# Kernel optimization log

Hardware: AMD Instinct MI355X
Metric: run time of the kernel (lower is better)

The kernel has to match this reference:

```python
import jax, jax.numpy as jnp
import numpy as np

N_NODES = 100000
N_EDGES = 1600000
D_IN = 128
D_OUT = 128
LN_EPS = 1e-5
MEAN_EPS = 1e-8


def setup_inputs() -> dict:
    key = jax.random.key(0)
    ks = jax.random.split(key, 8)
    x = jax.random.normal(ks[0], (N_NODES, D_IN), dtype=jnp.float32)
    edge_index = jax.random.randint(ks[1], (2, N_EDGES), 0, N_NODES, dtype=jnp.int64)
    s = 1.0 / np.sqrt(D_IN)
    W_agg = jax.random.uniform(ks[2], (D_OUT, D_IN), jnp.float32, -s, s)
    b_agg = jax.random.uniform(ks[3], (D_OUT,), jnp.float32, -s, s)
    W_self = jax.random.uniform(ks[4], (D_OUT, D_IN), jnp.float32, -s, s)
    b_self = jax.random.uniform(ks[5], (D_OUT,), jnp.float32, -s, s)
    gamma = jnp.ones((D_OUT,), jnp.float32)
    beta = jnp.zeros((D_OUT,), jnp.float32)
    return {"x": x, "edge_index": edge_index, "W_agg": W_agg, "b_agg": b_agg,
            "W_self": W_self, "b_self": b_self, "gamma": gamma, "beta": beta}


def reference(x, edge_index, W_agg, b_agg, W_self, b_self, gamma, beta):
    row, col = edge_index[0], edge_index[1]
    num_nodes = x.shape[0]
    # self path: Linear(in, out)
    self_out = x @ W_self.T + b_self                              # [N, D_OUT]
    # mean aggregation: fused gather + segment-sum (no index_add buffer passes)
    neighbor_sum = jax.ops.segment_sum(x[col], row, num_segments=num_nodes)   # [N, D_IN]
    ones = jnp.ones((col.shape[0], 1), dtype=x.dtype)
    neighbor_count = jax.ops.segment_sum(ones, row, num_segments=num_nodes)   # [N, 1]
    neighbor_mean = neighbor_sum / (neighbor_count + MEAN_EPS)
    agg_out = neighbor_mean @ W_agg.T + b_agg                     # [N, D_OUT]
    # relu -> LayerNorm (dropout is identity at eval)
    h = jax.nn.relu(self_out + agg_out)
    mu = jnp.mean(h, axis=-1, keepdims=True)
    var = jnp.mean(jnp.square(h - mu), axis=-1, keepdims=True)
    return (h - mu) * jax.lax.rsqrt(var + LN_EPS) * gamma + beta
```

## Files before the change

kernel.cpp:

```cpp
#include <hip/hip_runtime.h>

#define N_NODES 100000
#define N_EDGES 1600000
#define D 128
#define RPB 64
#define NBUCKET 1563
#define NBLK 196
#define EPB 8192
#define AGG_CAP 2048
#define XCB 3125
#define SCAN_PAD 1792

constexpr float LN_EPS   = 1e-5f;
constexpr float MEAN_EPS = 1e-8f;

typedef __attribute__((ext_vector_type(8))) short bf16x8;
typedef __attribute__((ext_vector_type(4))) float f32x4;
typedef __attribute__((ext_vector_type(2))) float f32x2;
typedef __attribute__((ext_vector_type(4))) unsigned uint4e;
typedef __attribute__((ext_vector_type(2))) unsigned uint2e;

__device__ inline unsigned short f2bf(float f) {
  union { float f; unsigned u; } v; v.f = f;
  return (unsigned short)((v.u + 0x7FFFu + ((v.u >> 16) & 1u)) >> 16);
}
__device__ inline unsigned pack2(float a, float b) {
  return (unsigned)f2bf(a) | ((unsigned)f2bf(b) << 16);
}

__global__ __launch_bounds__(256) void prep_sort(
    const float* __restrict__ x, const int* __restrict__ ei,
    const float* __restrict__ Wself, const float* __restrict__ Wagg,
    const float* __restrict__ bself, const float* __restrict__ bagg,
    unsigned short* __restrict__ xb, unsigned char* __restrict__ x8,
    unsigned short* __restrict__ wcat, float* __restrict__ bsum,
    unsigned* __restrict__ ent_sorted, int* __restrict__ chunkoff) {
  __shared__ int ent_s[EPB];
  __shared__ int cnt_s[SCAN_PAD];
  __shared__ int off_s[SCAN_PAD];
  __shared__ int sb[256];
  const int bid = blockIdx.x;
  const int t = threadIdx.x;

  if (bid < NBLK) {
    const int ebase = bid * EPB;
    const int nch = min(EPB, N_EDGES - ebase);
    const int base4 = bid * (EPB / 4);
    const int end4 = base4 + (nch >> 2);

    for (int i = t; i < SCAN_PAD; i += 256) cnt_s[i] = 0;
    __syncthreads();

#pragma unroll
    for (int k = 0; k < EPB / 1024; ++k) {
      int i4 = base4 + k * 256 + t;
      if (i4 < end4) {
        int4 r = ((const int4*)ei)[i4];
        atomicAdd(&cnt_s[r.x >> 6], 1);
        atomicAdd(&cnt_s[r.y >> 6], 1);
        atomicAdd(&cnt_s[r.z >> 6], 1);
        atomicAdd(&cnt_s[r.w >> 6], 1);
      }
    }
    __syncthreads();

    int psum = 0;
#pragma unroll
    for (int i = 0; i < 7; ++i) psum += cnt_s[t * 7 + i];
    sb[t] = psum;
    __syncthreads();
    for (int off = 1; off < 256; off <<= 1) {
      int u = (t >= off) ? sb[t - off] : 0;
      __syncthreads();
      sb[t] += u;
      __syncthreads();
    }
    int run = sb[t] - psum;
#pragma unroll
    for (int i = 0; i < 7; ++i) {
      off_s[t * 7 + i] = run;
      run += cnt_s[t * 7 + i];
    }
    __syncthreads();

    for (int b = t; b < NBUCKET; b += 256)
      chunkoff[b * NBLK + bid] = off_s[b] | (cnt_s[b] << 14);
    __syncthreads();

#pragma unroll
    for (int k = 0; k < EPB / 1024; ++k) {
      int i4 = base4 + k * 256 + t;
      if (i4 < end4) {
        int4 r = ((const int4*)ei)[i4];
        int4 c = ((const int4*)(ei + N_EDGES))[i4];
        int p0 = atomicAdd(&off_s[r.x >> 6], 1);
        ent_s[p0] = ((r.x & 63) << 17) | c.x;
        int p1 = atomicAdd(&off_s[r.y >> 6], 1);
        ent_s[p1] = ((r.y & 63) << 17) | c.y;
        int p2 = atomicAdd(&off_s[r.z >> 6], 1);
        ent_s[p2] = ((r.z & 63) << 17) | c.z;
        int p3 = atomicAdd(&off_s[r.w >> 6], 1);
        ent_s[p3] = ((r.w & 63) << 17) | c.w;
      }
    }
    __syncthreads();

    for (int i = t; i < nch; i += 256)
      ent_sorted[ebase + i] = (unsigned)ent_s[i];
  } else if (bid < NBLK + XCB) {
    const int f = (bid - NBLK) * 4096 + t * 16;
    const float4 v0 = ((const float4*)x)[(f >> 2) + 0];
    const float4 v1 = ((const float4*)x)[(f >> 2) + 1];
    const float4 v2 = ((const float4*)x)[(f >> 2) + 2];
    const float4 v3 = ((const float4*)x)[(f >> 2) + 3];
    uint4e lo, hi;
    lo.x = pack2(v0.x, v0.y); lo.y = pack2(v0.z, v0.w);
    lo.z = pack2(v1.x, v1.y); lo.w = pack2(v1.z, v1.w);
    hi.x = pack2(v2.x, v2.y); hi.y = pack2(v2.z, v2.w);
    hi.z = pack2(v3.x, v3.y); hi.w = pack2(v3.z, v3.w);
    *(uint4e*)(xb + f) = lo;
    *(uint4e*)(xb + f + 8) = hi;
    unsigned q0 = 0, q1 = 0, q2 = 0, q3 = 0;
    q0 = __builtin_amdgcn_cvt_pk_fp8_f32(v0.x, v0.y, q0, false);
    q0 = __builtin_amdgcn_cvt_pk_fp8_f32(v0.z, v0.w, q0, true);
    q1 = __builtin_amdgcn_cvt_pk_fp8_f32(v1.x, v1.y, q1, false);
    q1 = __builtin_amdgcn_cvt_pk_fp8_f32(v1.z, v1.w, q1, true);
    q2 = __builtin_amdgcn_cvt_pk_fp8_f32(v2.x, v2.y, q2, false);
    q2 = __builtin_amdgcn_cvt_pk_fp8_f32(v2.z, v2.w, q2, true);
    q3 = __builtin_amdgcn_cvt_pk_fp8_f32(v3.x, v3.y, q3, false);
    q3 = __builtin_amdgcn_cvt_pk_fp8_f32(v3.z, v3.w, q3, true);
    uint4e q; q.x = q0; q.y = q1; q.z = q2; q.w = q3;
    *(uint4e*)(x8 + f) = q;
  } else {
    const int blk = bid - NBLK - XCB;
#pragma unroll
    for (int k = 0; k < 8; ++k) {
      int idx = blk * 2048 + k * 256 + t;
      int o = idx >> 8, kc = idx & 255;
      float v = (kc < 128) ? Wself[o * 128 + kc] : Wagg[o * 128 + (kc - 128)];
      wcat[o * 256 + kc] = f2bf(v);
    }
    if (blk == 0 && t < 128) bsum[t] = bself[t] + bagg[t];
    if (blk == 0 && t < 32)
      *(unsigned*)(x8 + (size_t)N_NODES * 128 + t * 4) = 0u;
  }
}

__global__ __launch_bounds__(256) void aggregate(
    const unsigned char* __restrict__ x8, const unsigned* __restrict__ ent_sorted,
    const int* __restrict__ chunkoff, float* out) {
  __shared__ int ent_s[AGG_CAP];
  __shared__ int col_s[AGG_CAP];
  __shared__ int cnt_s[RPB];
  __shared__ int off_s[RPB];
  __shared__ int cur_s[RPB];
  __shared__ int wsum[4];

  const int b = blockIdx.x;
  const int t = threadIdx.x;
  const int w = t >> 6, lane = t & 63;

  int beg = 0, len = 0;
  if (t < NBLK) {
    int pk = chunkoff[b * NBLK + t];
    beg = pk & 16383;
    len = pk >> 14;
  }
  int v = len;
#pragma unroll
  for (int off = 1; off < 64; off <<= 1) {
    int u = __shfl_up(v, off, 64);
    if (lane >= off) v += u;
  }
  if (lane == 63) wsum[w] = v;
  if (t < RPB) cnt_s[t] = 0;
  __syncthreads();
  int pre = 0;
  for (int i = 0; i < w; ++i) pre += wsum[i];
  int n = wsum[0] + wsum[1] + wsum[2] + wsum[3];
  if (n > AGG_CAP) n = AGG_CAP;
  int dst = pre + v - len;
  if (t < NBLK) {
    const unsigned* src = ent_sorted + t * EPB + beg;
    for (int i = 0; i < len; ++i)
      if (dst + i < AGG_CAP) ent_s[dst + i] = (int)src[i];
  }
  __syncthreads();

  for (int i = t; i < n; i += 256) atomicAdd(&cnt_s[ent_s[i] >> 17], 1);
  __syncthreads();

  if (t < RPB) {
    int c = cnt_s[t];
    int sv = c;
#pragma unroll
    for (int off = 1; off < 64; off <<= 1) {
      int u = __shfl_up(sv, off, 64);
      if (t >= off) sv += u;
    }
    off_s[t] = sv - c;
    cur_s[t] = sv - c;
  }
  __syncthreads();

  for (int i = t; i < n; i += 256) {
    int e = ent_s[i];
    int pos = atomicAdd(&cur_s[e >> 17], 1);
    col_s[pos] = e & 0x1FFFF;
  }
  __syncthreads();

  const int half = lane >> 5, lq = lane & 31;
  const int nodebase = b << 6;
  for (int r0 = w; r0 < 32; r0 += 4) {
    const int rA = r0, rB = r0 + 32;
    const int begA = off_s[rA], degA = cnt_s[rA];
    const int begB = off_s[rB], degB = cnt_s[rB];
    const int dmax = max(degA, degB);
    float aA0 = 0.f, aA1 = 0.f, aA2 = 0.f, aA3 = 0.f;
    float aB0 = 0.f, aB1 = 0.f, aB2 = 0.f, aB3 = 0.f;
    for (int j0 = 0; j0 < dmax; j0 += 16) {
      unsigned pA[8], pB[8];
#pragma unroll
      for (int u = 0; u < 8; ++u) {
        int idx = j0 + u * 2 + half;
        int cA = col_s[(begA + idx) & (AGG_CAP - 1)];
        cA = (idx < degA) ? cA : N_NODES;
        pA[u] = *(const unsigned*)(x8 + (size_t)cA * 128 + lq * 4);
        int cB = col_s[(begB + idx) & (AGG_CAP - 1)];
        cB = (idx < degB) ? cB : N_NODES;
        pB[u] = *(const unsigned*)(x8 + (size_t)cB * 128 + lq * 4);
      }
#pragma unroll
      for (int u = 0; u < 8; ++u) {
        f32x2 lo = __builtin_amdgcn_cvt_pk_f32_fp8(pA[u], false);
        f32x2 hi = __builtin_amdgcn_cvt_pk_f32_fp8(pA[u], true);
        aA0 += lo.x; aA1 += lo.y; aA2 += hi.x; aA3 += hi.y;
      }
#pragma unroll
      for (int u = 0; u < 8; ++u) {
        f32x2 lo = __builtin_amdgcn_cvt_pk_f32_fp8(pB[u], false);
        f32x2 hi = __builtin_amdgcn_cvt_pk_f32_fp8(pB[u], true);
        aB0 += lo.x; aB1 += lo.y; aB2 += hi.x; aB3 += hi.y;
      }
    }
    aA0 += __shfl_xor(aA0, 32, 64);
    aA1 += __shfl_xor(aA1, 32, 64);
    aA2 += __shfl_xor(aA2, 32, 64);
    aA3 += __shfl_xor(aA3, 32, 64);
    aB0 += __shfl_xor(aB0, 32, 64);
    aB1 += __shfl_xor(aB1, 32, 64);
    aB2 += __shfl_xor(aB2, 32, 64);
    aB3 += __shfl_xor(aB3, 32, 64);
    if (half == 0) {
      int nodeA = nodebase + rA;
      if (nodeA < N_NODES) {
        float inv = 1.0f / ((float)degA + MEAN_EPS);
        uint2e o;
        o.x = pack2(aA0 * inv, aA1 * inv);
        o.y = pack2(aA2 * inv, aA3 * inv);
        *(uint2e*)((unsigned short*)(out + (size_t)nodeA * D) + lq * 4) = o;
      }
      int nodeB = nodebase + rB;
      if (nodeB < N_NODES) {
        float inv = 1.0f / ((float)degB + MEAN_EPS);
        uint2e o;
        o.x = pack2(aB0 * inv, aB1 * inv);
        o.y = pack2(aB2 * inv, aB3 * inv);
        *(uint2e*)((unsigned short*)(out + (size_t)nodeB * D) + lq * 4) = o;
      }
    }
  }
}

__global__ __launch_bounds__(512, 4) void gemm_mfma_ln(
    const unsigned short* __restrict__ xb, const float* out_mean,
    const unsigned short* __restrict__ wcat, const float* __restrict__ bsum,
    const float* __restrict__ gamma, const float* __restrict__ beta,
    float* out) {
  __shared__ unsigned short Bs[128 * 264];
  __shared__ float bias_s[128];

  const int t = threadIdx.x;
  const int w = t >> 6, lane = t & 63;
  const int q = lane >> 4, s = lane & 15;
  const int base = blockIdx.x * 128;

  if (t < 128) bias_s[t] = bsum[t];

#pragma unroll
  for (int r = 0; r < 8; ++r) {
    int f = r * 512 + t;
    int row = f >> 5, c = f & 31;
    uint4 v = *(const uint4*)(wcat + row * 256 + c * 8);
    *(uint4*)(Bs + row * 264 + c * 8) = v;
  }

  const int arow = base + w * 16 + s;
  const int asafe = (arow < N_NODES) ? arow : 0;
  const unsigned short* xrow = xb + (size_t)asafe * 128;
  const unsigned short* mrow = (const unsigned short*)(out_mean + (size_t)asafe * 128);
  bf16x8 a[8];
#pragma unroll
  for (int kk = 0; kk < 4; ++kk)
    a[kk] = *(const bf16x8*)(xrow + kk * 32 + q * 8);
#pragma unroll
  for (int kk = 0; kk < 4; ++kk)
    a[4 + kk] = *(const bf16x8*)(mrow + kk * 32 + q * 8);

  __syncthreads();

  f32x4 acc[8];
#pragma unroll
  for (int j = 0; j < 8; ++j) acc[j] = (f32x4)(0.0f);

#pragma unroll
  for (int kk = 0; kk < 8; ++kk) {
    const int ko = kk * 32 + q * 8;
#pragma unroll
    for (int j = 0; j < 8; ++j) {
      bf16x8 bv = *(const bf16x8*)(Bs + (j * 16 + s) * 264 + ko);
      acc[j] = __builtin_amdgcn_mfma_f32_16x16x32_bf16(a[kk], bv, acc[j], 0, 0, 0);
    }
  }

#pragma unroll
  for (int j = 0; j < 8; ++j) {
    float bb = bias_s[j * 16 + s];
#pragma unroll
    for (int r = 0; r < 4; ++r)
      acc[j][r] = fmaxf(acc[j][r] + bb, 0.0f);
  }

  float g[8], be[8];
#pragma unroll
  for (int j = 0; j < 8; ++j) {
    g[j]  = gamma[j * 16 + s];
    be[j] = beta[j * 16 + s];
  }

#pragma unroll
  for (int r = 0; r < 4; ++r) {
    float s1 = 0.f, s2 = 0.f;
#pragma unroll
    for (int j = 0; j < 8; ++j) {
      float h = acc[j][r];
      s1 += h; s2 += h * h;
    }
#pragma unroll
    for (int m = 1; m < 16; m <<= 1) {
      s1 += __shfl_xor(s1, m, 64);
      s2 += __shfl_xor(s2, m, 64);
    }
    int node = base + w * 16 + q * 4 + r;
    if (node < N_NODES) {
      float mu = s1 * (1.0f / 128.0f);
      float var = s2 * (1.0f / 128.0f) - mu * mu;
      float rstd = rsqrtf(var + LN_EPS);
      float* orow = out + (size_t)node * 128;
#pragma unroll
      for (int j = 0; j < 8; ++j)
        orow[j * 16 + s] = (acc[j][r] - mu) * rstd * g[j] + be[j];
    }
  }
}

extern "C" void kernel_launch(void* const* d_in, const int* in_sizes, int n_in,
                              void* d_out, int out_size, void* d_ws, size_t ws_size,
                              hipStream_t stream) {
  const float* x     = (const float*)d_in[0];
  const int*   ei    = (const int*)d_in[1];
  const float* Wagg  = (const float*)d_in[2];
  const float* bagg  = (const float*)d_in[3];
  const float* Wself = (const float*)d_in[4];
  const float* bself = (const float*)d_in[5];
  const float* gamma = (const float*)d_in[6];
  const float* beta  = (const float*)d_in[7];
  float* out = (float*)d_out;

  unsigned short* xb   = (unsigned short*)d_ws;
  unsigned char*  x8   = (unsigned char*)(xb + (size_t)N_NODES * D);
  unsigned short* wcat = (unsigned short*)(x8 + (size_t)(N_NODES + 1) * D);
  float* bsum      = (float*)(wcat + 128 * 256);
  unsigned* ent_sorted = (unsigned*)(bsum + 128);
  int* chunkoff    = (int*)(ent_sorted + (size_t)NBLK * EPB);

  prep_sort<<<NBLK + XCB + 16, 256, 0, stream>>>(
      x, ei, Wself, Wagg, bself, bagg, xb, x8, wcat, bsum, ent_sorted, chunkoff);

  aggregate<<<NBUCKET, 256, 0, stream>>>(x8, ent_sorted, chunkoff, out);

  gemm_mfma_ln<<<(N_NODES + 127) / 128, 512, 0, stream>>>(
      xb, out, wcat, bsum, gamma, beta, out);
}
```

Before: 213.3 us.

## Drop bf16 copy of x and widen aggregate to 512 threads, one row per wave

The bf16 copy of x is no longer written in the prep kernel. The GEMM kernel now reads fp32 x directly and converts it to bf16 in registers, which saves a 25.6MB write and read round trip. The aggregate kernel moves to 512 threads with 8 waves, each wave processing one node row at a time. Each lane gathers 8 fp8 bytes over 4 edges per iteration, followed by a 4-way shuffle reduction. The trade-off is that the GEMM reads twice as many bytes for the x half, and the aggregate kernel has fewer rows in flight per wave.

```diff
diff --git a/kernel.cpp b/kernel.cpp
--- a/kernel.cpp
+++ b/kernel.cpp
@@ -32,7 +32,7 @@
     const float* __restrict__ x, const int* __restrict__ ei,
     const float* __restrict__ Wself, const float* __restrict__ Wagg,
     const float* __restrict__ bself, const float* __restrict__ bagg,
-    unsigned short* __restrict__ xb, unsigned char* __restrict__ x8,
+    unsigned char* __restrict__ x8,
     unsigned short* __restrict__ wcat, float* __restrict__ bsum,
     unsigned* __restrict__ ent_sorted, int* __restrict__ chunkoff) {
   __shared__ int ent_s[EPB];
@@ -113,13 +113,6 @@
     const float4 v1 = ((const float4*)x)[(f >> 2) + 1];
     const float4 v2 = ((const float4*)x)[(f >> 2) + 2];
     const float4 v3 = ((const float4*)x)[(f >> 2) + 3];
-    uint4e lo, hi;
-    lo.x = pack2(v0.x, v0.y); lo.y = pack2(v0.z, v0.w);
-    lo.z = pack2(v1.x, v1.y); lo.w = pack2(v1.z, v1.w);
-    hi.x = pack2(v2.x, v2.y); hi.y = pack2(v2.z, v2.w);
-    hi.z = pack2(v3.x, v3.y); hi.w = pack2(v3.z, v3.w);
-    *(uint4e*)(xb + f) = lo;
-    *(uint4e*)(xb + f + 8) = hi;
     unsigned q0 = 0, q1 = 0, q2 = 0, q3 = 0;
     q0 = __builtin_amdgcn_cvt_pk_fp8_f32(v0.x, v0.y, q0, false);
     q0 = __builtin_amdgcn_cvt_pk_fp8_f32(v0.z, v0.w, q0, true);
@@ -146,7 +139,7 @@
   }
 }
 
-__global__ __launch_bounds__(256) void aggregate(
+__global__ __launch_bounds__(512, 6) void aggregate(
     const unsigned char* __restrict__ x8, const unsigned* __restrict__ ent_sorted,
     const int* __restrict__ chunkoff, float* out) {
   __shared__ int ent_s[AGG_CAP];
@@ -172,22 +165,22 @@
     int u = __shfl_up(v, off, 64);
     if (lane >= off) v += u;
   }
-  if (lane == 63) wsum[w] = v;
+  if (w < 4 && lane == 63) wsum[w] = v;
   if (t < RPB) cnt_s[t] = 0;
   __syncthreads();
-  int pre = 0;
-  for (int i = 0; i < w; ++i) pre += wsum[i];
   int n = wsum[0] + wsum[1] + wsum[2] + wsum[3];
   if (n > AGG_CAP) n = AGG_CAP;
-  int dst = pre + v - len;
   if (t < NBLK) {
+    int pre = 0;
+    for (int i = 0; i < w; ++i) pre += wsum[i];
+    int dst = pre + v - len;
     const unsigned* src = ent_sorted + t * EPB + beg;
     for (int i = 0; i < len; ++i)
       if (dst + i < AGG_CAP) ent_s[dst + i] = (int)src[i];
   }
   __syncthreads();
 
-  for (int i = t; i < n; i += 256) atomicAdd(&cnt_s[ent_s[i] >> 17], 1);
+  for (int i = t; i < n; i += 512) atomicAdd(&cnt_s[ent_s[i] >> 17], 1);
   __syncthreads();
 
   if (t < RPB) {
@@ -203,78 +196,63 @@
   }
   __syncthreads();
 
-  for (int i = t; i < n; i += 256) {
+  for (int i = t; i < n; i += 512) {
     int e = ent_s[i];
     int pos = atomicAdd(&cur_s[e >> 17], 1);
     col_s[pos] = e & 0x1FFFF;
   }
   __syncthreads();
 
-  const int half = lane >> 5, lq = lane & 31;
+  const int e4 = lane >> 4, lq = lane & 15;
   const int nodebase = b << 6;
-  for (int r0 = w; r0 < 32; r0 += 4) {
-    const int rA = r0, rB = r0 + 32;
-    const int begA = off_s[rA], degA = cnt_s[rA];
-    const int begB = off_s[rB], degB = cnt_s[rB];
-    const int dmax = max(degA, degB);
-    float aA0 = 0.f, aA1 = 0.f, aA2 = 0.f, aA3 = 0.f;
-    float aB0 = 0.f, aB1 = 0.f, aB2 = 0.f, aB3 = 0.f;
-    for (int j0 = 0; j0 < dmax; j0 += 16) {
-      unsigned pA[8], pB[8];
-#pragma unroll
-      for (int u = 0; u < 8; ++u) {
-        int idx = j0 + u * 2 + half;
-        int cA = col_s[(begA + idx) & (AGG_CAP - 1)];
-        cA = (idx < degA) ? cA : N_NODES;
-        pA[u] = *(const unsigned*)(x8 + (size_t)cA * 128 + lq * 4);
-        int cB = col_s[(begB + idx) & (AGG_CAP - 1)];
-        cB = (idx < degB) ? cB : N_NODES;
-        pB[u] = *(const unsigned*)(x8 + (size_t)cB * 128 + lq * 4);
+  for (int lr = w; lr < RPB; lr += 8) {
+    int node = nodebase + lr;
+    if (node >= N_NODES) break;
+    int rbeg = off_s[lr];
+    int deg = cnt_s[lr];
+    float a0 = 0.f, a1 = 0.f, a2 = 0.f, a3 = 0.f;
+    float a4 = 0.f, a5 = 0.f, a6 = 0.f, a7 = 0.f;
+    for (int j0 = 0; j0 < deg; j0 += 16) {
+      uint2e p[4];
+#pragma unroll
+      for (int u = 0; u < 4; ++u) {
+        int idx = j0 + u * 4 + e4;
+        int col = col_s[(rbeg + idx) & (AGG_CAP - 1)];
+        col = (idx < deg) ? col : N_NODES;
+        p[u] = *(const uint2e*)(x8 + (size_t)col * 128 + lq * 8);
       }
 #pragma unroll
-      for (int u = 0; u < 8; ++u) {
-        f32x2 lo = __builtin_amdgcn_cvt_pk_f32_fp8(pA[u], false);
-        f32x2 hi = __builtin_amdgcn_cvt_pk_f32_fp8(pA[u], true);
-        aA0 += lo.x; aA1 += lo.y; aA2 += hi.x; aA3 += hi.y;
+      for (int u = 0; u < 4; ++u) {
+        f32x2 l0 = __builtin_amdgcn_cvt_pk_f32_fp8(p[u].x, false);
+        f32x2 h0 = __builtin_amdgcn_cvt_pk_f32_fp8(p[u].x, true);
+        f32x2 l1 = __builtin_amdgcn_cvt_pk_f32_fp8(p[u].y, false);
+        f32x2 h1 = __builtin_amdgcn_cvt_pk_f32_fp8(p[u].y, true);
+        a0 += l0.x; a1 += l0.y; a2 += h0.x; a3 += h0.y;
+        a4 += l1.x; a5 += l1.y; a6 += h1.x; a7 += h1.y;
       }
-#pragma unroll
-      for (int u = 0; u < 8; ++u) {
-        f32x2 lo = __builtin_amdgcn_cvt_pk_f32_fp8(pB[u], false);
-        f32x2 hi = __builtin_amdgcn_cvt_pk_f32_fp8(pB[u], true);
-        aB0 += lo.x; aB1 += lo.y; aB2 += hi.x; aB3 += hi.y;
-      }
-    }
-    aA0 += __shfl_xor(aA0, 32, 64);
-    aA1 += __shfl_xor(aA1, 32, 64);
-    aA2 += __shfl_xor(aA2, 32, 64);
-    aA3 += __shfl_xor(aA3, 32, 64);
-    aB0 += __shfl_xor(aB0, 32, 64);
-    aB1 += __shfl_xor(aB1, 32, 64);
-    aB2 += __shfl_xor(aB2, 32, 64);
-    aB3 += __shfl_xor(aB3, 32, 64);
-    if (half == 0) {
-      int nodeA = nodebase + rA;
-      if (nodeA < N_NODES) {
-        float inv = 1.0f / ((float)degA + MEAN_EPS);
-        uint2e o;
-        o.x = pack2(aA0 * inv, aA1 * inv);
-        o.y = pack2(aA2 * inv, aA3 * inv);
-        *(uint2e*)((unsigned short*)(out + (size_t)nodeA * D) + lq * 4) = o;
-      }
-      int nodeB = nodebase + rB;
-      if (nodeB < N_NODES) {
-        float inv = 1.0f / ((float)degB + MEAN_EPS);
-        uint2e o;
-        o.x = pack2(aB0 * inv, aB1 * inv);
-        o.y = pack2(aB2 * inv, aB3 * inv);
-        *(uint2e*)((unsigned short*)(out + (size_t)nodeB * D) + lq * 4) = o;
-      }
+    }
+    a0 += __shfl_xor(a0, 16, 64); a0 += __shfl_xor(a0, 32, 64);
+    a1 += __shfl_xor(a1, 16, 64); a1 += __shfl_xor(a1, 32, 64);
+    a2 += __shfl_xor(a2, 16, 64); a2 += __shfl_xor(a2, 32, 64);
+    a3 += __shfl_xor(a3, 16, 64); a3 += __shfl_xor(a3, 32, 64);
+    a4 += __shfl_xor(a4, 16, 64); a4 += __shfl_xor(a4, 32, 64);
+    a5 += __shfl_xor(a5, 16, 64); a5 += __shfl_xor(a5, 32, 64);
+    a6 += __shfl_xor(a6, 16, 64); a6 += __shfl_xor(a6, 32, 64);
+    a7 += __shfl_xor(a7, 16, 64); a7 += __shfl_xor(a7, 32, 64);
+    if (lane < 16) {
+      float inv = 1.0f / ((float)deg + MEAN_EPS);
+      uint4e o;
+      o.x = pack2(a0 * inv, a1 * inv);
+      o.y = pack2(a2 * inv, a3 * inv);
+      o.z = pack2(a4 * inv, a5 * inv);
+      o.w = pack2(a6 * inv, a7 * inv);
+      *(uint4e*)((unsigned short*)(out + (size_t)node * D) + lq * 8) = o;
     }
   }
 }
 
 __global__ __launch_bounds__(512, 4) void gemm_mfma_ln(
-    const unsigned short* __restrict__ xb, const float* out_mean,
+    const float* __restrict__ x, const float* out_mean,
     const unsigned short* __restrict__ wcat, const float* __restrict__ bsum,
     const float* __restrict__ gamma, const float* __restrict__ beta,
     float* out) {
@@ -298,12 +276,20 @@
 
   const int arow = base + w * 16 + s;
   const int asafe = (arow < N_NODES) ? arow : 0;
-  const unsigned short* xrow = xb + (size_t)asafe * 128;
+  const float* xrow = x + (size_t)asafe * 128;
   const unsigned short* mrow = (const unsigned short*)(out_mean + (size_t)asafe * 128);
   bf16x8 a[8];
 #pragma unroll
-  for (int kk = 0; kk < 4; ++kk)
-    a[kk] = *(const bf16x8*)(xrow + kk * 32 + q * 8);
+  for (int kk = 0; kk < 4; ++kk) {
+    const float4 f0 = *(const float4*)(xrow + kk * 32 + q * 8);
+    const float4 f1 = *(const float4*)(xrow + kk * 32 + q * 8 + 4);
+    bf16x8 av;
+    av[0] = (short)f2bf(f0.x); av[1] = (short)f2bf(f0.y);
+    av[2] = (short)f2bf(f0.z); av[3] = (short)f2bf(f0.w);
+    av[4] = (short)f2bf(f1.x); av[5] = (short)f2bf(f1.y);
+    av[6] = (short)f2bf(f1.z); av[7] = (short)f2bf(f1.w);
+    a[kk] = av;
+  }
 #pragma unroll
   for (int kk = 0; kk < 4; ++kk)
     a[4 + kk] = *(const bf16x8*)(mrow + kk * 32 + q * 8);
@@ -378,18 +364,17 @@
   const float* beta  = (const float*)d_in[7];
   float* out = (float*)d_out;
 
-  unsigned short* xb   = (unsigned short*)d_ws;
-  unsigned char*  x8   = (unsigned char*)(xb + (size_t)N_NODES * D);
+  unsigned char*  x8   = (unsigned char*)d_ws;
   unsigned short* wcat = (unsigned short*)(x8 + (size_t)(N_NODES + 1) * D);
   float* bsum      = (float*)(wcat + 128 * 256);
   unsigned* ent_sorted = (unsigned*)(bsum + 128);
   int* chunkoff    = (int*)(ent_sorted + (size_t)NBLK * EPB);
 
   prep_sort<<<NBLK + XCB + 16, 256, 0, stream>>>(
-      x, ei, Wself, Wagg, bself, bagg, xb, x8, wcat, bsum, ent_sorted, chunkoff);
-
-  aggregate<<<NBUCKET, 256, 0, stream>>>(x8, ent_sorted, chunkoff, out);
+      x, ei, Wself, Wagg, bself, bagg, x8, wcat, bsum, ent_sorted, chunkoff);
+
+  aggregate<<<NBUCKET, 512, 0, stream>>>(x8, ent_sorted, chunkoff, out);
 
   gemm_mfma_ln<<<(N_NODES + 127) / 128, 512, 0, stream>>>(
-      xb, out, wcat, bsum, gamma, beta, out);
-}
+      x, out, wcat, bsum, gamma, beta, out);
+}
```

Measured after the change: 201.0 us. -5.8%, faster.
